# Optimization experiments

Hardware: AMD Instinct MI355X
Metric: run time of the kernel (lower is better)

Reference implementation:

```python
import jax, jax.numpy as jnp
import numpy as np

N, C, H, W = 4, 64, 64, 64
K = 3


def _unfold(x, k):
    """torch F.unfold with padding k//2: [n,c,h,w] -> [n, c*k*k, h*w].
    Feature ordering matches torch: index = c*k*k + i*k + j."""
    p = k // 2
    n, c, h, w = x.shape
    xp = jnp.pad(x, ((0, 0), (0, 0), (p, p), (p, p)))
    patches = jnp.stack(
        [xp[:, :, i:i + h, j:j + w] for i in range(k) for j in range(k)], axis=2
    )  # [n, c, k*k, h, w]
    return patches.reshape(n, c * k * k, h * w)


def _mask_vec(c, k):
    # causal patch mask from __init__: zero out center-and-right of middle row and all rows below
    m = np.ones((c, k, k), np.float32)
    m[:, k // 2, k // 2:] = 0
    m[:, k // 2 + 1:, :] = 0
    return jnp.asarray(m.reshape(1, c * k * k, 1))


def setup_inputs() -> dict:
    key = jax.random.key(0)
    k1, k2 = jax.random.split(key)
    y_hat = jax.random.normal(k1, (N, C, H, W), dtype=jnp.float32)
    y_prob = jax.random.uniform(k2, (N, 1, H, W), dtype=jnp.float32)
    return {"y_hat": y_hat, "y_prob": y_prob}


def reference(y_hat, y_prob):
    k = K
    n, c, h, w = y_hat.shape
    L = h * w
    mask = _mask_vec(c, k)

    u = _unfold(y_hat, k) * mask                              # [n, c*k*k, L]
    u = u / jnp.maximum(jnp.linalg.norm(u, axis=1, keepdims=True), 1e-12)
    R = jnp.einsum('nfl,nfm->nlm', u, u)                      # [n, L, L] cosine sims

    # eval path: keep strictly-upper triangle (causal: l < m)
    row = jnp.arange(L)[:, None]
    col = jnp.arange(L)[None, :]
    R = jnp.where(col > row, R, 0.0)

    R_star = jnp.max(R, axis=1)                               # [n, L]
    arg = jnp.argmax(R, axis=1).astype(jnp.int32)             # [n, L]

    y_unf = _unfold(y_hat, k)                                 # [n, c*k*k, L]
    ref_unfold = jnp.take_along_axis(y_unf, arg[:, None, :], axis=2)

    prob_unf = y_prob.reshape(n, -1, L)                       # 1x1 unfold
    U_unf = jnp.take_along_axis(prob_unf, arg[:, None, :], axis=2)

    S = R_star.reshape(n, 1, h, w)
    U = U_unf.reshape(n, -1, h, w)

    # eval-mode position-0 overrides
    S = S.at[:, :, 0, 0].set(1e-8)
    U = U.at[:, :, 0, 0].set(1e-8)
    ref_unfold = ref_unfold.at[:, :, 0].set(0.0)
    arg = arg.at[:, 0].set(-1)

    S = jnp.clip(S, 1e-8, 1.0)
    U = jnp.clip(U, 1e-8, 1.0)
    return S, U, ref_unfold, arg
```

## Files before the change

### kernel.cpp

```cpp
#include <hip/hip_runtime.h>
#include <stdint.h>

#define Nn 4
#define Cc 64
#define LL 4096
#define KK 256
#define TRI2 528

typedef _Float16 half8 __attribute__((ext_vector_type(8)));
typedef float f32x16 __attribute__((ext_vector_type(16)));
typedef float f4a __attribute__((ext_vector_type(4), aligned(4)));

__device__ __forceinline__ unsigned f2ord(float f) {
    unsigned u = __float_as_uint(f);
    return u ^ ((u & 0x80000000u) ? 0xFFFFFFFFu : 0x80000000u);
}
__device__ __forceinline__ float ord2f(unsigned o) {
    unsigned u = (o & 0x80000000u) ? (o ^ 0x80000000u) : ~o;
    return __uint_as_float(u);
}
__device__ __forceinline__ unsigned short h2u(_Float16 h) {
    union { _Float16 f; unsigned short u; } x; x.f = h; return x.u;
}

__global__ __launch_bounds__(256) void build_v(const float* __restrict__ yhat,
                                               unsigned short* __restrict__ VhT,
                                               unsigned short* __restrict__ VlT,
                                               unsigned long long* __restrict__ best) {
    int blk = blockIdx.x;
    int xcd = blk & 7;
    int n = xcd >> 1;
    int i64 = (blk >> 3) + (xcd & 1) * 128;
    int tid = threadIdx.x;
    if (tid < 16) best[(size_t)n * LL + i64 * 16 + tid] = 0ull;

    int cg = tid & 15;
    int l = i64 * 16 + (tid >> 4);
    int y = l >> 6, x = l & 63;
    const float* src = yhat + (size_t)n * (Cc * LL);

    float vals[16];
    float sumsq = 0.f;
#pragma unroll
    for (int ci = 0; ci < 4; ++ci) {
        const float* p = src + (cg * 4 + ci) * LL;
        float t0 = (y > 0 && x > 0)  ? p[l - 65] : 0.f;
        float t1 = (y > 0)           ? p[l - 64] : 0.f;
        float t2 = (y > 0 && x < 63) ? p[l - 63] : 0.f;
        float t3 = (x > 0)           ? p[l - 1]  : 0.f;
        vals[ci * 4 + 0] = t0; vals[ci * 4 + 1] = t1;
        vals[ci * 4 + 2] = t2; vals[ci * 4 + 3] = t3;
        sumsq += t0 * t0 + t1 * t1 + t2 * t2 + t3 * t3;
    }
    sumsq += __shfl_xor(sumsq, 1, 64);
    sumsq += __shfl_xor(sumsq, 2, 64);
    sumsq += __shfl_xor(sumsq, 4, 64);
    sumsq += __shfl_xor(sumsq, 8, 64);
    float inv = 1.f / fmaxf(sqrtf(sumsq), 1e-12f);

    size_t nl = (size_t)n * LL + l;
    unsigned short* dh = VhT + nl * KK + cg * 16;
    unsigned short* dl = VlT + nl * KK + cg * 16;
#pragma unroll
    for (int ci = 0; ci < 4; ++ci) {
        ushort4 hv, lv;
        unsigned short* ph = &hv.x;
        unsigned short* pl = &lv.x;
#pragma unroll
        for (int tp = 0; tp < 4; ++tp) {
            float v = vals[ci * 4 + tp] * inv;
            _Float16 h = (fabsf(v) < 6.1035e-5f) ? (_Float16)0 : (_Float16)v;
            _Float16 lo = (_Float16)((v - (float)h) * 2048.0f);
            ph[tp] = h2u(h * (_Float16)2048.0f);
            pl[tp] = h2u(lo);
        }
        *(ushort4*)(dh + ci * 4) = hv;
        *(ushort4*)(dl + ci * 4) = lv;
    }
}

__global__ __launch_bounds__(256) void simmax(const unsigned short* __restrict__ Vh,
                                              const unsigned short* __restrict__ Vl,
                                              unsigned long long* __restrict__ best) {
    __shared__ __align__(16) unsigned short S[16384];

    int bx = blockIdx.x;
    int xcd = bx & 7, idx = bx >> 3;
    int n = xcd >> 1;
    int t = (xcd & 1) * 264 + idx;
    int j = (int)((sqrtf(8.f * (float)t + 1.f) - 1.f) * 0.5f);
    while ((j + 1) * (j + 2) / 2 <= t) ++j;
    while (j * (j + 1) / 2 > t) --j;
    int i = t - j * (j + 1) / 2;
    int l0 = i * 128, m0 = j * 128;

    const unsigned short* VhB = Vh + (size_t)n * (LL * KK);
    const unsigned short* VlB = Vl + (size_t)n * (LL * KK);

    int tid = threadIdx.x;
    int w = tid >> 6, lane = tid & 63;
    int r5 = lane & 31, h5 = lane >> 5;
    int rw = (w & 1) * 64;
    int cw = (w >> 1) * 64;
    bool skip = (i == j) && (rw == 64) && (cw == 0);

    f32x16 acc[2][2];
#pragma unroll
    for (int r = 0; r < 2; ++r)
#pragma unroll
        for (int c = 0; c < 2; ++c) acc[r][c] = (f32x16)0.f;

    int srow = tid >> 2;
    int scl = tid & 3;
    int sp = (scl ^ ((srow >> 1) & 3)) * 8;
    int shg = scl * 8;

    int sfr = (r5 >> 1) & 3;

    for (int k0 = 0; k0 < KK; k0 += 32) {
        const size_t ra = (size_t)(l0 + srow) * KK + k0 + shg;
        const size_t rb = (size_t)(l0 + 64 + srow) * KK + k0 + shg;
        const size_t rc = (size_t)(m0 + srow) * KK + k0 + shg;
        const size_t rd = (size_t)(m0 + 64 + srow) * KK + k0 + shg;
        uint4 ah0 = *(const uint4*)(VhB + ra);
        uint4 ah1 = *(const uint4*)(VhB + rb);
        uint4 al0 = *(const uint4*)(VlB + ra);
        uint4 al1 = *(const uint4*)(VlB + rb);
        uint4 bh0 = *(const uint4*)(VhB + rc);
        uint4 bh1 = *(const uint4*)(VhB + rd);
        uint4 bl0 = *(const uint4*)(VlB + rc);
        uint4 bl1 = *(const uint4*)(VlB + rd);
        __syncthreads();
        *(uint4*)&S[srow * 32 + sp]                 = ah0;
        *(uint4*)&S[(64 + srow) * 32 + sp]          = ah1;
        *(uint4*)&S[4096 + srow * 32 + sp]          = al0;
        *(uint4*)&S[4096 + (64 + srow) * 32 + sp]   = al1;
        *(uint4*)&S[8192 + srow * 32 + sp]          = bh0;
        *(uint4*)&S[8192 + (64 + srow) * 32 + sp]   = bh1;
        *(uint4*)&S[12288 + srow * 32 + sp]         = bl0;
        *(uint4*)&S[12288 + (64 + srow) * 32 + sp]  = bl1;
        __syncthreads();
        if (!skip) {
            half8 fah[2][2], fal[2][2], fbh[2][2], fbl[2][2];
#pragma unroll
            for (int r = 0; r < 2; ++r)
#pragma unroll
                for (int kc = 0; kc < 2; ++kc) {
                    int pc = ((kc * 2 + h5) ^ sfr) * 8;
                    int ao = (rw + r * 32 + r5) * 32 + pc;
                    int bo = (cw + r * 32 + r5) * 32 + pc;
                    fah[r][kc] = *(half8*)&S[ao];
                    fal[r][kc] = *(half8*)&S[4096 + ao];
                    fbh[r][kc] = *(half8*)&S[8192 + bo];
                    fbl[r][kc] = *(half8*)&S[12288 + bo];
                }
#pragma unroll
            for (int kc = 0; kc < 2; ++kc)
#pragma unroll
                for (int r = 0; r < 2; ++r)
#pragma unroll
                    for (int c = 0; c < 2; ++c)
                        acc[r][c] = __builtin_amdgcn_mfma_f32_32x32x16_f16(fal[r][kc], fbh[c][kc], acc[r][c], 0, 0, 0);
#pragma unroll
            for (int kc = 0; kc < 2; ++kc)
#pragma unroll
                for (int r = 0; r < 2; ++r)
#pragma unroll
                    for (int c = 0; c < 2; ++c)
                        acc[r][c] = __builtin_amdgcn_mfma_f32_32x32x16_f16(fah[r][kc], fbl[c][kc], acc[r][c], 0, 0, 0);
#pragma unroll
            for (int kc = 0; kc < 2; ++kc)
#pragma unroll
                for (int r = 0; r < 2; ++r)
#pragma unroll
                    for (int c = 0; c < 2; ++c)
                        acc[r][c] = __builtin_amdgcn_mfma_f32_32x32x16_f16(fah[r][kc], fbh[c][kc], acc[r][c], 0, 0, 0);
        }
    }

    if (skip) return;
    unsigned long long* bb = best + (size_t)n * LL;
    const float s = 1.f / 4194304.f;
#pragma unroll
    for (int c = 0; c < 2; ++c) {
        int m = m0 + cw + c * 32 + r5;
        unsigned long long key = 0ull;
#pragma unroll
        for (int r = 0; r < 2; ++r)
#pragma unroll
            for (int g = 0; g < 16; ++g) {
                int l = l0 + rw + r * 32 + (g & 3) + 8 * (g >> 2) + 4 * h5;
                if (l < m) {
                    float v = acc[r][c][g] * s;
                    unsigned long long k2 =
                        ((unsigned long long)f2ord(v) << 32) |
                        (unsigned long long)(0xFFFFFFFFu - (unsigned)l);
                    key = (k2 > key) ? k2 : key;
                }
            }
        unsigned long long o = __shfl_xor(key, 32, 64);
        key = (o > key) ? o : key;
        if (h5 == 0 && key != 0ull) atomicMax(bb + m, key);
    }
}

__global__ __launch_bounds__(256) void writeout(const float* __restrict__ yhat,
                                                const float* __restrict__ yprob,
                                                const unsigned long long* __restrict__ best,
                                                float* __restrict__ out) {
    int blk = blockIdx.x;
    int xcd = blk & 7;
    int n = xcd >> 1;
    int idx = (blk >> 3) + (xcd & 1) * 512;
    int mb = idx >> 4;
    int fc = idx & 15;
    int tid = threadIdx.x;
    int mm = tid & 63;
    int fs = tid >> 6;
    int c = fc * 4 + fs;
    int m = mb * 64 + mm;

    unsigned long long key = best[(size_t)n * LL + m];
    unsigned l = 0xFFFFFFFFu - (unsigned)(key & 0xFFFFFFFFull);
    float val = ord2f((unsigned)(key >> 32));
    bool zero = (m == 0);
    if (zero) l = 0;
    int ly = (int)(l >> 6), lx = (int)(l & 63);

    float* Sout = out;
    float* Uout = out + 16384;
    float* Rout = out + 32768;
    float* Aout = out + 9469952;

    if (fc == 0 && fs == 0) {
        float S = zero ? 1e-8f : fminf(fmaxf(val, 1e-8f), 1.0f);
        float U = zero ? 1e-8f : fminf(fmaxf(yprob[(size_t)n * LL + l], 1e-8f), 1.0f);
        Sout[(size_t)n * LL + m] = S;
        Uout[(size_t)n * LL + m] = U;
        Aout[(size_t)n * LL + m] = zero ? -1.0f : (float)l;
    }

    const float* src = yhat + (size_t)n * (Cc * LL);
    const float* plane = src + (size_t)c * LL;
    float* dst = Rout + (size_t)n * (576 * LL) + m;
    bool fast = (!zero) && (lx >= 1) && (lx <= 61);
#pragma unroll
    for (int r3 = 0; r3 < 3; ++r3) {
        int yy = ly + r3 - 1;
        bool rowok = (!zero) && (yy >= 0) && (yy < 64);
        float t0 = 0.f, t1 = 0.f, t2 = 0.f;
        if (rowok) {
            if (fast) {
                f4a v = *(const f4a*)(plane + yy * 64 + lx - 1);
                t0 = v.x; t1 = v.y; t2 = v.z;
            } else {
                if (lx > 0)  t0 = plane[yy * 64 + lx - 1];
                t1 = plane[yy * 64 + lx];
                if (lx < 63) t2 = plane[yy * 64 + lx + 1];
            }
        }
        size_t f = (size_t)(c * 9 + r3 * 3) * LL;
        __builtin_nontemporal_store(t0, dst + f);
        __builtin_nontemporal_store(t1, dst + f + LL);
        __builtin_nontemporal_store(t2, dst + f + 2 * (size_t)LL);
    }
}

extern "C" void kernel_launch(void* const* d_in, const int* in_sizes, int n_in,
                              void* d_out, int out_size, void* d_ws, size_t ws_size,
                              hipStream_t stream) {
    const float* yhat  = (const float*)d_in[0];
    const float* yprob = (const float*)d_in[1];
    float* out = (float*)d_out;

    unsigned short* VhT = (unsigned short*)d_ws;
    unsigned short* VlT = (unsigned short*)((char*)d_ws + 8388608);
    unsigned long long* best =
        (unsigned long long*)((char*)d_ws + 16777216);

    build_v<<<1024, 256, 0, stream>>>(yhat, VhT, VlT, best);
    simmax<<<Nn * TRI2, 256, 0, stream>>>(VhT, VlT, best);
    writeout<<<4096, 256, 0, stream>>>(yhat, yprob, best, out);
}
```

Measured before the change: 154.6 us.

## Load low-half fragments directly from global in MFMA layout and double-buffer high half

```diff
diff --git a/kernel.cpp b/kernel.cpp
--- a/kernel.cpp
+++ b/kernel.cpp
@@ -60,7 +60,7 @@
 
     size_t nl = (size_t)n * LL + l;
     unsigned short* dh = VhT + nl * KK + cg * 16;
-    unsigned short* dl = VlT + nl * KK + cg * 16;
+    unsigned short* dl = VlT + ((((size_t)n * 128 + (l >> 5)) * 16 + cg) << 9) + (l & 31) * 8;
 #pragma unroll
     for (int ci = 0; ci < 4; ++ci) {
         ushort4 hv, lv;
@@ -75,7 +75,7 @@
             pl[tp] = h2u(lo);
         }
         *(ushort4*)(dh + ci * 4) = hv;
-        *(ushort4*)(dl + ci * 4) = lv;
+        *(ushort4*)(dl + (ci >> 1) * 256 + (ci & 1) * 4) = lv;
     }
 }
 
@@ -114,46 +114,64 @@
     int scl = tid & 3;
     int sp = (scl ^ ((srow >> 1) & 3)) * 8;
     int shg = scl * 8;
-
     int sfr = (r5 >> 1) & 3;
 
-    for (int k0 = 0; k0 < KK; k0 += 32) {
-        const size_t ra = (size_t)(l0 + srow) * KK + k0 + shg;
-        const size_t rb = (size_t)(l0 + 64 + srow) * KK + k0 + shg;
-        const size_t rc = (size_t)(m0 + srow) * KK + k0 + shg;
-        const size_t rd = (size_t)(m0 + 64 + srow) * KK + k0 + shg;
-        uint4 ah0 = *(const uint4*)(VhB + ra);
-        uint4 ah1 = *(const uint4*)(VhB + rb);
-        uint4 al0 = *(const uint4*)(VlB + ra);
-        uint4 al1 = *(const uint4*)(VlB + rb);
-        uint4 bh0 = *(const uint4*)(VhB + rc);
-        uint4 bh1 = *(const uint4*)(VhB + rd);
-        uint4 bl0 = *(const uint4*)(VlB + rc);
-        uint4 bl1 = *(const uint4*)(VlB + rd);
-        __syncthreads();
-        *(uint4*)&S[srow * 32 + sp]                 = ah0;
-        *(uint4*)&S[(64 + srow) * 32 + sp]          = ah1;
-        *(uint4*)&S[4096 + srow * 32 + sp]          = al0;
-        *(uint4*)&S[4096 + (64 + srow) * 32 + sp]   = al1;
-        *(uint4*)&S[8192 + srow * 32 + sp]          = bh0;
-        *(uint4*)&S[8192 + (64 + srow) * 32 + sp]   = bh1;
-        *(uint4*)&S[12288 + srow * 32 + sp]         = bl0;
-        *(uint4*)&S[12288 + (64 + srow) * 32 + sp]  = bl1;
-        __syncthreads();
+    const unsigned short* loA = VlB + ((size_t)((l0 + rw) >> 5) << 13) + lane * 8;
+    const unsigned short* loB = VlB + ((size_t)((m0 + cw) >> 5) << 13) + lane * 8;
+
+    {
+        uint4 a0 = *(const uint4*)(VhB + (size_t)(l0 + srow) * KK + shg);
+        uint4 a1 = *(const uint4*)(VhB + (size_t)(l0 + 64 + srow) * KK + shg);
+        uint4 b0 = *(const uint4*)(VhB + (size_t)(m0 + srow) * KK + shg);
+        uint4 b1 = *(const uint4*)(VhB + (size_t)(m0 + 64 + srow) * KK + shg);
+        *(uint4*)&S[srow * 32 + sp]               = a0;
+        *(uint4*)&S[(64 + srow) * 32 + sp]        = a1;
+        *(uint4*)&S[4096 + srow * 32 + sp]        = b0;
+        *(uint4*)&S[4096 + (64 + srow) * 32 + sp] = b1;
+    }
+    __syncthreads();
+
+#pragma unroll
+    for (int kt = 0; kt < 8; ++kt) {
+        const int k0 = kt * 32;
+        const int kb = kt * 2;
+        const int cur = (kt & 1) * 8192;
+        const int nxt = 8192 - cur;
+
+        half8 fal[2][2], fbl[2][2];
         if (!skip) {
-            half8 fah[2][2], fal[2][2], fbh[2][2], fbl[2][2];
+#pragma unroll
+            for (int kc = 0; kc < 2; ++kc)
+#pragma unroll
+                for (int r = 0; r < 2; ++r)
+                    fal[r][kc] = *(const half8*)(loA + ((r * 16 + kb + kc) << 9));
+#pragma unroll
+            for (int kc = 0; kc < 2; ++kc)
+#pragma unroll
+                for (int r = 0; r < 2; ++r)
+                    fbl[r][kc] = *(const half8*)(loB + ((r * 16 + kb + kc) << 9));
+        }
+
+        uint4 na0, na1, nb0, nb1;
+        if (kt < 7) {
+            const int kn = k0 + 32;
+            na0 = *(const uint4*)(VhB + (size_t)(l0 + srow) * KK + kn + shg);
+            na1 = *(const uint4*)(VhB + (size_t)(l0 + 64 + srow) * KK + kn + shg);
+            nb0 = *(const uint4*)(VhB + (size_t)(m0 + srow) * KK + kn + shg);
+            nb1 = *(const uint4*)(VhB + (size_t)(m0 + 64 + srow) * KK + kn + shg);
+        }
+
+        if (!skip) {
+            half8 fah[2][2], fbh[2][2];
 #pragma unroll
             for (int r = 0; r < 2; ++r)
 #pragma unroll
                 for (int kc = 0; kc < 2; ++kc) {
                     int pc = ((kc * 2 + h5) ^ sfr) * 8;
-                    int ao = (rw + r * 32 + r5) * 32 + pc;
-                    int bo = (cw + r * 32 + r5) * 32 + pc;
-                    fah[r][kc] = *(half8*)&S[ao];
-                    fal[r][kc] = *(half8*)&S[4096 + ao];
-                    fbh[r][kc] = *(half8*)&S[8192 + bo];
-                    fbl[r][kc] = *(half8*)&S[12288 + bo];
+                    fbh[r][kc] = *(half8*)&S[cur + 4096 + (cw + r * 32 + r5) * 32 + pc];
+                    fah[r][kc] = *(half8*)&S[cur + (rw + r * 32 + r5) * 32 + pc];
                 }
+            __builtin_amdgcn_s_setprio(1);
 #pragma unroll
             for (int kc = 0; kc < 2; ++kc)
 #pragma unroll
@@ -175,6 +193,15 @@
 #pragma unroll
                     for (int c = 0; c < 2; ++c)
                         acc[r][c] = __builtin_amdgcn_mfma_f32_32x32x16_f16(fah[r][kc], fbh[c][kc], acc[r][c], 0, 0, 0);
+            __builtin_amdgcn_s_setprio(0);
+        }
+
+        if (kt < 7) {
+            *(uint4*)&S[nxt + srow * 32 + sp]               = na0;
+            *(uint4*)&S[nxt + (64 + srow) * 32 + sp]        = na1;
+            *(uint4*)&S[nxt + 4096 + srow * 32 + sp]        = nb0;
+            *(uint4*)&S[nxt + 4096 + (64 + srow) * 32 + sp] = nb1;
+            __syncthreads();
         }
     }
 
```

Measured after the change: 154.5 us. Within noise of the previous version (-0.1%).

## Pre-pack V into MFMA fragment layout and load fragments directly from global

Applied to the files above, without the earlier changes.

```diff
diff --git a/kernel.cpp b/kernel.cpp
--- a/kernel.cpp
+++ b/kernel.cpp
@@ -10,6 +10,7 @@
 typedef _Float16 half8 __attribute__((ext_vector_type(8)));
 typedef float f32x16 __attribute__((ext_vector_type(16)));
 typedef float f4a __attribute__((ext_vector_type(4), aligned(4)));
+typedef unsigned short ushort8v __attribute__((ext_vector_type(8)));
 
 __device__ __forceinline__ unsigned f2ord(float f) {
     unsigned u = __float_as_uint(f);
@@ -58,32 +59,29 @@
     sumsq += __shfl_xor(sumsq, 8, 64);
     float inv = 1.f / fmaxf(sqrtf(sumsq), 1e-12f);
 
-    size_t nl = (size_t)n * LL + l;
-    unsigned short* dh = VhT + nl * KK + cg * 16;
-    unsigned short* dl = VlT + nl * KK + cg * 16;
-#pragma unroll
-    for (int ci = 0; ci < 4; ++ci) {
-        ushort4 hv, lv;
-        unsigned short* ph = &hv.x;
-        unsigned short* pl = &lv.x;
-#pragma unroll
-        for (int tp = 0; tp < 4; ++tp) {
-            float v = vals[ci * 4 + tp] * inv;
-            _Float16 h = (fabsf(v) < 6.1035e-5f) ? (_Float16)0 : (_Float16)v;
-            _Float16 lo = (_Float16)((v - (float)h) * 2048.0f);
-            ph[tp] = h2u(h * (_Float16)2048.0f);
-            pl[tp] = h2u(lo);
-        }
-        *(ushort4*)(dh + ci * 4) = hv;
-        *(ushort4*)(dl + ci * 4) = lv;
-    }
+    size_t pk = ((((size_t)n * 128 + (l >> 5)) * 16 + cg) << 9) + (l & 31) * 8;
+    unsigned short* dh = VhT + pk;
+    unsigned short* dl = VlT + pk;
+    ushort8v hA, hB, lA, lB;
+#pragma unroll
+    for (int kk = 0; kk < 16; ++kk) {
+        float v = vals[kk] * inv;
+        _Float16 h = (fabsf(v) < 6.1035e-5f) ? (_Float16)0 : (_Float16)v;
+        _Float16 lo = (_Float16)((v - (float)h) * 2048.0f);
+        unsigned short hu = h2u(h * (_Float16)2048.0f);
+        unsigned short lu = h2u(lo);
+        if (kk < 8) { hA[kk] = hu; lA[kk] = lu; }
+        else        { hB[kk - 8] = hu; lB[kk - 8] = lu; }
+    }
+    *(ushort8v*)(dh)       = hA;
+    *(ushort8v*)(dh + 256) = hB;
+    *(ushort8v*)(dl)       = lA;
+    *(ushort8v*)(dl + 256) = lB;
 }
 
 __global__ __launch_bounds__(256) void simmax(const unsigned short* __restrict__ Vh,
                                               const unsigned short* __restrict__ Vl,
                                               unsigned long long* __restrict__ best) {
-    __shared__ __align__(16) unsigned short S[16384];
-
     int bx = blockIdx.x;
     int xcd = bx & 7, idx = bx >> 3;
     int n = xcd >> 1;
@@ -94,15 +92,20 @@
     int i = t - j * (j + 1) / 2;
     int l0 = i * 128, m0 = j * 128;
 
-    const unsigned short* VhB = Vh + (size_t)n * (LL * KK);
-    const unsigned short* VlB = Vl + (size_t)n * (LL * KK);
-
     int tid = threadIdx.x;
     int w = tid >> 6, lane = tid & 63;
     int r5 = lane & 31, h5 = lane >> 5;
     int rw = (w & 1) * 64;
     int cw = (w >> 1) * 64;
-    bool skip = (i == j) && (rw == 64) && (cw == 0);
+    if ((i == j) && (rw == 64) && (cw == 0)) return;
+
+    const unsigned short* VhB = Vh + (size_t)n * (LL * KK);
+    const unsigned short* VlB = Vl + (size_t)n * (LL * KK);
+
+    const unsigned short* A_hi = VhB + ((size_t)((l0 + rw) >> 5) << 13) + lane * 8;
+    const unsigned short* A_lo = VlB + ((size_t)((l0 + rw) >> 5) << 13) + lane * 8;
+    const unsigned short* B_hi = VhB + ((size_t)((m0 + cw) >> 5) << 13) + lane * 8;
+    const unsigned short* B_lo = VlB + ((size_t)((m0 + cw) >> 5) << 13) + lane * 8;
 
     f32x16 acc[2][2];
 #pragma unroll
@@ -110,75 +113,49 @@
 #pragma unroll
         for (int c = 0; c < 2; ++c) acc[r][c] = (f32x16)0.f;
 
-    int srow = tid >> 2;
-    int scl = tid & 3;
-    int sp = (scl ^ ((srow >> 1) & 3)) * 8;
-    int shg = scl * 8;
-
-    int sfr = (r5 >> 1) & 3;
-
-    for (int k0 = 0; k0 < KK; k0 += 32) {
-        const size_t ra = (size_t)(l0 + srow) * KK + k0 + shg;
-        const size_t rb = (size_t)(l0 + 64 + srow) * KK + k0 + shg;
-        const size_t rc = (size_t)(m0 + srow) * KK + k0 + shg;
-        const size_t rd = (size_t)(m0 + 64 + srow) * KK + k0 + shg;
-        uint4 ah0 = *(const uint4*)(VhB + ra);
-        uint4 ah1 = *(const uint4*)(VhB + rb);
-        uint4 al0 = *(const uint4*)(VlB + ra);
-        uint4 al1 = *(const uint4*)(VlB + rb);
-        uint4 bh0 = *(const uint4*)(VhB + rc);
-        uint4 bh1 = *(const uint4*)(VhB + rd);
-        uint4 bl0 = *(const uint4*)(VlB + rc);
-        uint4 bl1 = *(const uint4*)(VlB + rd);
-        __syncthreads();
-        *(uint4*)&S[srow * 32 + sp]                 = ah0;
-        *(uint4*)&S[(64 + srow) * 32 + sp]          = ah1;
-        *(uint4*)&S[4096 + srow * 32 + sp]          = al0;
-        *(uint4*)&S[4096 + (64 + srow) * 32 + sp]   = al1;
-        *(uint4*)&S[8192 + srow * 32 + sp]          = bh0;
-        *(uint4*)&S[8192 + (64 + srow) * 32 + sp]   = bh1;
-        *(uint4*)&S[12288 + srow * 32 + sp]         = bl0;
-        *(uint4*)&S[12288 + (64 + srow) * 32 + sp]  = bl1;
-        __syncthreads();
-        if (!skip) {
-            half8 fah[2][2], fal[2][2], fbh[2][2], fbl[2][2];
+#pragma unroll 1
+    for (int kb = 0; kb < 16; kb += 2) {
+        half8 fal[2][2], fah[2][2], fbl[2][2], fbh[2][2];
+#pragma unroll
+        for (int kc = 0; kc < 2; ++kc)
+#pragma unroll
+            for (int r = 0; r < 2; ++r) {
+                fal[r][kc] = *(const half8*)(A_lo + ((r * 16 + kb + kc) << 9));
+                fbh[r][kc] = *(const half8*)(B_hi + ((r * 16 + kb + kc) << 9));
+            }
+#pragma unroll
+        for (int kc = 0; kc < 2; ++kc)
+#pragma unroll
+            for (int r = 0; r < 2; ++r) {
+                fah[r][kc] = *(const half8*)(A_hi + ((r * 16 + kb + kc) << 9));
+                fbl[r][kc] = *(const half8*)(B_lo + ((r * 16 + kb + kc) << 9));
+            }
+
+        __builtin_amdgcn_s_setprio(1);
+#pragma unroll
+        for (int kc = 0; kc < 2; ++kc)
 #pragma unroll
             for (int r = 0; r < 2; ++r)
 #pragma unroll
-                for (int kc = 0; kc < 2; ++kc) {
-                    int pc = ((kc * 2 + h5) ^ sfr) * 8;
-                    int ao = (rw + r * 32 + r5) * 32 + pc;
-                    int bo = (cw + r * 32 + r5) * 32 + pc;
-                    fah[r][kc] = *(half8*)&S[ao];
-                    fal[r][kc] = *(half8*)&S[4096 + ao];
-                    fbh[r][kc] = *(half8*)&S[8192 + bo];
-                    fbl[r][kc] = *(half8*)&S[12288 + bo];
-                }
-#pragma unroll
-            for (int kc = 0; kc < 2; ++kc)
-#pragma unroll
-                for (int r = 0; r < 2; ++r)
-#pragma unroll
-                    for (int c = 0; c < 2; ++c)
-                        acc[r][c] = __builtin_amdgcn_mfma_f32_32x32x16_f16(fal[r][kc], fbh[c][kc], acc[r][c], 0, 0, 0);
-#pragma unroll
-            for (int kc = 0; kc < 2; ++kc)
-#pragma unroll
-                for (int r = 0; r < 2; ++r)
-#pragma unroll
-                    for (int c = 0; c < 2; ++c)
-                        acc[r][c] = __builtin_amdgcn_mfma_f32_32x32x16_f16(fah[r][kc], fbl[c][kc], acc[r][c], 0, 0, 0);
-#pragma unroll
-            for (int kc = 0; kc < 2; ++kc)
-#pragma unroll
-                for (int r = 0; r < 2; ++r)
-#pragma unroll
-                    for (int c = 0; c < 2; ++c)
-                        acc[r][c] = __builtin_amdgcn_mfma_f32_32x32x16_f16(fah[r][kc], fbh[c][kc], acc[r][c], 0, 0, 0);
-        }
-    }
-
-    if (skip) return;
+                for (int c = 0; c < 2; ++c)
+                    acc[r][c] = __builtin_amdgcn_mfma_f32_32x32x16_f16(fal[r][kc], fbh[c][kc], acc[r][c], 0, 0, 0);
+#pragma unroll
+        for (int kc = 0; kc < 2; ++kc)
+#pragma unroll
+            for (int r = 0; r < 2; ++r)
+#pragma unroll
+                for (int c = 0; c < 2; ++c)
+                    acc[r][c] = __builtin_amdgcn_mfma_f32_32x32x16_f16(fah[r][kc], fbl[c][kc], acc[r][c], 0, 0, 0);
+#pragma unroll
+        for (int kc = 0; kc < 2; ++kc)
+#pragma unroll
+            for (int r = 0; r < 2; ++r)
+#pragma unroll
+                for (int c = 0; c < 2; ++c)
+                    acc[r][c] = __builtin_amdgcn_mfma_f32_32x32x16_f16(fah[r][kc], fbh[c][kc], acc[r][c], 0, 0, 0);
+        __builtin_amdgcn_s_setprio(0);
+    }
+
     unsigned long long* bb = best + (size_t)n * LL;
     const float s = 1.f / 4194304.f;
 #pragma unroll
```

Result: no change. 152.7 us (-1.3%).
